# Optimization experiments

Hardware: AMD Instinct MI355X
Metric: run time of the kernel (lower is better)

Reference implementation:

```python
import jax, jax.numpy as jnp
import numpy as np

B, S, H = 1, 2048, 4096
NH, DN, DR, DV = 32, 128, 64, 128   # heads, nope dim, rope dim, v dim
QK = DN + DR                         # 192
RQ, RKV = 1536, 512
EPS = 1e-6
NEG = jnp.float32(-1e9)


def rmsnorm(x, w, eps=EPS):
    x32 = x.astype(jnp.float32)
    var = jnp.mean(x32 * x32, axis=-1, keepdims=True)
    return (x32 * jax.lax.rsqrt(var + eps)).astype(x.dtype) * w


def rope_complex(x, cos, sin):
    # x: [..., S, D]; interpret adjacent pairs as complex, multiply by e^{i*theta}
    xr, xi = x[..., 0::2], x[..., 1::2]
    or_ = xr * cos - xi * sin
    oi_ = xr * sin + xi * cos
    return jnp.stack([or_, oi_], axis=-1).reshape(x.shape)


def setup_inputs() -> dict:
    key = jax.random.key(0)
    ks = jax.random.split(key, 8)
    std = 0.02
    # RoPE angles: theta_j = pos * base^{-2j/DR}, shape [B, S, DR/2]
    inv_freq = 1.0 / (10000.0 ** (np.arange(0, DR, 2, dtype=np.float32) / DR))
    pos = np.arange(S, dtype=np.float32)
    freqs = jnp.asarray(np.broadcast_to(pos[:, None] * inv_freq[None, :], (B, S, DR // 2)))
    return {
        "hidden_states": jax.random.normal(ks[0], (B, S, H), jnp.float32),
        "freqs": freqs,
        "q_a_w": jax.random.normal(ks[1], (RQ, H), jnp.float32) * std,
        "q_a_ln_w": jnp.ones((RQ,), jnp.float32),
        "q_b_w": jax.random.normal(ks[2], (NH * QK, RQ), jnp.float32) * std,
        "kv_a_w": jax.random.normal(ks[3], (RKV + DR, H), jnp.float32) * std,
        "kv_a_ln_w": jnp.ones((RKV,), jnp.float32),
        "kv_b_w": jax.random.normal(ks[4], (NH * (DN + DV), RKV), jnp.float32) * std,
        "o_w": jax.random.normal(ks[5], (H, NH * DV), jnp.float32) * std,
    }


def reference(hidden_states, freqs, q_a_w, q_a_ln_w, q_b_w, kv_a_w, kv_a_ln_w, kv_b_w, o_w):
    b, s, _ = hidden_states.shape
    # --- low-rank Q: hidden -> q_lora_rank -> heads*(nope+rope) ---
    q = rmsnorm(hidden_states @ q_a_w.T, q_a_ln_w) @ q_b_w.T          # [B,S,NH*QK]
    q = q.reshape(b, s, NH, QK).transpose(0, 2, 1, 3)                  # [B,NH,S,QK]
    q_pass, q_rot = q[..., :DN], q[..., DN:]                           # [B,NH,S,DN],[B,NH,S,DR]
    # --- compressed KV + shared rope key ---
    ckv = hidden_states @ kv_a_w.T                                     # [B,S,RKV+DR]
    k_pass_c, k_rot = ckv[..., :RKV], ckv[..., RKV:]
    kv = rmsnorm(k_pass_c, kv_a_ln_w) @ kv_b_w.T                       # [B,S,NH*(DN+DV)]
    kv = kv.reshape(b, s, NH, DN + DV).transpose(0, 2, 1, 3)           # [B,NH,S,DN+DV]
    k_pass, v = kv[..., :DN], kv[..., DN:]
    k_rot = k_rot.reshape(b, 1, s, DR)                                 # [B,1,S,DR]
    # --- decoupled RoPE (complex form) ---
    cos = jnp.cos(freqs)[:, None]                                      # [B,1,S,DR/2]
    sin = jnp.sin(freqs)[:, None]
    q_rot = rope_complex(q_rot, cos, sin)
    k_rot = rope_complex(k_rot, cos, sin)
    k_rot = jnp.broadcast_to(k_rot, (b, NH, s, DR))
    query = jnp.concatenate([q_pass, q_rot], axis=-1)                  # [B,NH,S,QK]
    key = jnp.concatenate([k_pass, k_rot], axis=-1)
    # --- causal attention ---
    scaling = QK ** -0.5
    scores = jnp.einsum("bhqd,bhkd->bhqk", query, key) * scaling
    causal = jnp.tril(jnp.ones((s, s), bool))
    scores = jnp.where(causal, scores, NEG)
    probs = jax.nn.softmax(scores.astype(jnp.float32), axis=-1).astype(query.dtype)
    out = jnp.einsum("bhqk,bhkd->bhqd", probs, v)                      # [B,NH,S,DV]
    out = out.transpose(0, 2, 1, 3).reshape(b, s, NH * DV)
    return out @ o_w.T                                                 # [B,S,H]
```

## Files before the change

### kernel.cpp

```cpp
#include <hip/hip_runtime.h>
#define S_LEN 2048
#define HDIM 4096
#define NHEAD 32
#define QKD 192
#define RQ_ 1536
#define CKV_W 576
#define NQKV 2112
#define KVW 8192
#define QFW 6144
#define SC2F 0.1041216313667742f

typedef float f32x4 __attribute__((ext_vector_type(4)));
typedef __bf16 bf16x8 __attribute__((ext_vector_type(8)));

__device__ __forceinline__ unsigned short f2bf(float f) {
  unsigned int u = __float_as_uint(f);
  u += 0x7fffu + ((u >> 16) & 1u);
  return (unsigned short)(u >> 16);
}
__device__ __forceinline__ float b2f(unsigned short u) {
  return __uint_as_float((unsigned int)u << 16);
}
__device__ __forceinline__ float ex2(float x) { return exp2f(x); }

__device__ __forceinline__ void stage16(const void* g, void* lds_base, int lane) {
  __builtin_amdgcn_global_load_lds(
      (const __attribute__((address_space(1))) unsigned int*)g,
      (__attribute__((address_space(3))) unsigned int*)lds_base, 16, 0, 0);
}

__global__ __launch_bounds__(256) void cvt_kernel(
    const float* __restrict__ in, unsigned short* __restrict__ out, int n8) {
  int i = blockIdx.x * 256 + threadIdx.x;
  if (i >= n8) return;
  const float4* p = reinterpret_cast<const float4*>(in) + (size_t)i * 2;
  float4 a = p[0], b = p[1];
  unsigned long long lo = (unsigned long long)f2bf(a.x) | ((unsigned long long)f2bf(a.y) << 16)
      | ((unsigned long long)f2bf(a.z) << 32) | ((unsigned long long)f2bf(a.w) << 48);
  unsigned long long hi = (unsigned long long)f2bf(b.x) | ((unsigned long long)f2bf(b.y) << 16)
      | ((unsigned long long)f2bf(b.z) << 32) | ((unsigned long long)f2bf(b.w) << 48);
  unsigned long long* q = reinterpret_cast<unsigned long long*>(out) + (size_t)i * 2;
  q[0] = lo; q[1] = hi;
}

__global__ __launch_bounds__(256) void cvt2_kernel(
    const float* __restrict__ s1, int n8_1,
    const float* __restrict__ s2, unsigned short* __restrict__ out, int n8_tot) {
  int i = blockIdx.x * 256 + threadIdx.x;
  if (i >= n8_tot) return;
  const float4* p = (i < n8_1)
      ? reinterpret_cast<const float4*>(s1) + (size_t)i * 2
      : reinterpret_cast<const float4*>(s2) + (size_t)(i - n8_1) * 2;
  float4 a = p[0], b = p[1];
  unsigned long long lo = (unsigned long long)f2bf(a.x) | ((unsigned long long)f2bf(a.y) << 16)
      | ((unsigned long long)f2bf(a.z) << 32) | ((unsigned long long)f2bf(a.w) << 48);
  unsigned long long hi = (unsigned long long)f2bf(b.x) | ((unsigned long long)f2bf(b.y) << 16)
      | ((unsigned long long)f2bf(b.z) << 32) | ((unsigned long long)f2bf(b.w) << 48);
  unsigned long long* q = reinterpret_cast<unsigned long long*>(out) + (size_t)i * 2;
  q[0] = lo; q[1] = hi;
}

template<bool BF16OUT, bool SPLITK>
__global__ __launch_bounds__(256) void gemm_bf(
    const unsigned short* __restrict__ A, int lda,
    const unsigned short* __restrict__ B, int ldb,
    void* __restrict__ Cv, int ldc, int N, int K) {
  __shared__ unsigned short As[2][4][128][8];
  __shared__ unsigned short Bs[2][4][128][8];
  const int tid = threadIdx.x, lane = tid & 63, w = tid >> 6;
  const int gx = (int)gridDim.x, gy = (int)gridDim.y;
  const int nwg = gx * gy;
  int lin = (int)blockIdx.y * gx + (int)blockIdx.x;
  if ((nwg & 7) == 0) lin = (lin & 7) * (nwg >> 3) + (lin >> 3);
  const int bm = (lin % gy) * 128, bn = (lin / gy) * 128;
  const int koff = SPLITK ? (int)blockIdx.z * K : 0;
  const int wr = (w >> 1) * 64, wc = (w & 1) * 64;
  const int lg = lane >> 4, lm = lane & 15;
  f32x4 acc[4][4] = {};
  const int arow = bm + lane;
  int brow = bn + lane; if (brow >= N) brow = N - 1;

  auto STAGE = [&](int buf, int k0) {
#pragma unroll
    for (int i = 0; i < 2; ++i) {
      stage16(A + (size_t)(arow + i * 64) * lda + koff + k0 + w * 8, &As[buf][w][i * 64][0], lane);
      int br2 = brow + i * 64; if (br2 >= N) br2 = N - 1;
      stage16(B + (size_t)br2 * ldb + koff + k0 + w * 8, &Bs[buf][w][i * 64][0], lane);
    }
  };
  STAGE(0, 0);
  __syncthreads();
  int cur = 0;
  for (int k0 = 0; k0 < K; k0 += 32) {
    if (k0 + 32 < K) STAGE(cur ^ 1, k0 + 32);
    bf16x8 af[4], bf[4];
#pragma unroll
    for (int i = 0; i < 4; ++i)
      af[i] = *reinterpret_cast<const bf16x8*>(&As[cur][lg][wr + i * 16 + lm][0]);
#pragma unroll
    for (int j = 0; j < 4; ++j)
      bf[j] = *reinterpret_cast<const bf16x8*>(&Bs[cur][lg][wc + j * 16 + lm][0]);
    __builtin_amdgcn_s_setprio(1);
#pragma unroll
    for (int i = 0; i < 4; ++i)
#pragma unroll
      for (int j = 0; j < 4; ++j)
        acc[i][j] = __builtin_amdgcn_mfma_f32_16x16x32_bf16(af[i], bf[j], acc[i][j], 0, 0, 0);
    __builtin_amdgcn_s_setprio(0);
    __syncthreads();
    cur ^= 1;
  }
  size_t zoff = SPLITK ? (size_t)blockIdx.z * S_LEN * N : 0;
#pragma unroll
  for (int i = 0; i < 4; ++i)
#pragma unroll
    for (int j = 0; j < 4; ++j)
#pragma unroll
      for (int r = 0; r < 4; ++r) {
        int row = bm + wr + i * 16 + lg * 4 + r;
        int col = bn + wc + j * 16 + lm;
        if (col < N) {
          if constexpr (BF16OUT)
            ((unsigned short*)Cv)[(size_t)row * ldc + col] = f2bf(acc[i][j][r]);
          else
            ((float*)Cv)[zoff + (size_t)row * ldc + col] = acc[i][j][r];
        }
      }
}

__global__ __launch_bounds__(256) void gemm_dual(
    const unsigned short* __restrict__ A1, int lda1,
    const unsigned short* __restrict__ B1, int ldb1,
    unsigned short* __restrict__ C1, int ldc1, int K1, int nwg1,
    const unsigned short* __restrict__ A2, int lda2,
    const unsigned short* __restrict__ B2, int ldb2,
    unsigned short* __restrict__ C2, int ldc2, int K2,
    unsigned short* __restrict__ VtOut) {
  __shared__ unsigned short As[2][4][128][8];
  __shared__ unsigned short Bs[2][4][128][8];
  const int tid = threadIdx.x, lane = tid & 63, w = tid >> 6;
  const int raw = (int)blockIdx.x;
  const bool second = (raw >= nwg1);
  const int nwg = second ? ((int)gridDim.x - nwg1) : nwg1;
  int lin = second ? raw - nwg1 : raw;
  lin = (lin & 7) * (nwg >> 3) + (lin >> 3);
  const int gy = S_LEN / 128;
  const int bm = (lin % gy) * 128, bn = (lin / gy) * 128;
  const unsigned short* A = second ? A2 : A1;
  const unsigned short* B = second ? B2 : B1;
  unsigned short* C = second ? C2 : C1;
  const int lda = second ? lda2 : lda1;
  const int ldb = second ? ldb2 : ldb1;
  const int ldc = second ? ldc2 : ldc1;
  const int K = second ? K2 : K1;
  const int wr = (w >> 1) * 64, wc = (w & 1) * 64;
  const int lg = lane >> 4, lm = lane & 15;
  f32x4 acc[4][4] = {};
  const int arow = bm + lane;
  const int brow = bn + lane;

  auto STAGE = [&](int buf, int k0) {
#pragma unroll
    for (int i = 0; i < 2; ++i) {
      stage16(A + (size_t)(arow + i * 64) * lda + k0 + w * 8, &As[buf][w][i * 64][0], lane);
      stage16(B + (size_t)(brow + i * 64) * ldb + k0 + w * 8, &Bs[buf][w][i * 64][0], lane);
    }
  };
  STAGE(0, 0);
  __syncthreads();
  int cur = 0;
  for (int k0 = 0; k0 < K; k0 += 32) {
    if (k0 + 32 < K) STAGE(cur ^ 1, k0 + 32);
    bf16x8 af[4], bf[4];
#pragma unroll
    for (int i = 0; i < 4; ++i)
      af[i] = *reinterpret_cast<const bf16x8*>(&As[cur][lg][wr + i * 16 + lm][0]);
#pragma unroll
    for (int j = 0; j < 4; ++j)
      bf[j] = *reinterpret_cast<const bf16x8*>(&Bs[cur][lg][wc + j * 16 + lm][0]);
    __builtin_amdgcn_s_setprio(1);
#pragma unroll
    for (int i = 0; i < 4; ++i)
#pragma unroll
      for (int j = 0; j < 4; ++j)
        acc[i][j] = __builtin_amdgcn_mfma_f32_16x16x32_bf16(af[i], bf[j], acc[i][j], 0, 0, 0);
    __builtin_amdgcn_s_setprio(0);
    __syncthreads();
    cur ^= 1;
  }

  if (second && (bn & 128)) {
    const int h2 = bn >> 8;
#pragma unroll
    for (int i = 0; i < 4; ++i)
#pragma unroll
      for (int j = 0; j < 4; ++j) {
        int d = wc + j * 16 + lm;
        unsigned long long pk =
              (unsigned long long)f2bf(acc[i][j][0])
            | ((unsigned long long)f2bf(acc[i][j][1]) << 16)
            | ((unsigned long long)f2bf(acc[i][j][2]) << 32)
            | ((unsigned long long)f2bf(acc[i][j][3]) << 48);
        *reinterpret_cast<unsigned long long*>(
            VtOut + (size_t)(h2 * 128 + d) * S_LEN + bm + wr + i * 16 + lg * 4) = pk;
      }
    return;
  }
#pragma unroll
  for (int i = 0; i < 4; ++i)
#pragma unroll
    for (int j = 0; j < 4; ++j)
#pragma unroll
      for (int r = 0; r < 4; ++r) {
        int row = bm + wr + i * 16 + lg * 4 + r;
        int col = bn + wc + j * 16 + lm;
        C[(size_t)row * ldc + col] = f2bf(acc[i][j][r]);
      }
}

__global__ __launch_bounds__(256) void rms_fused(
    const float* __restrict__ P, const float* __restrict__ wq,
    const float* __restrict__ wkv, const float* __restrict__ freqs,
    unsigned short* __restrict__ yq, unsigned short* __restrict__ ykv,
    unsigned short* __restrict__ Kr) {
  __shared__ float red[8];
  const int row = blockIdx.x, tid = threadIdx.x;
  const float* base = P + (size_t)row * NQKV;
  float xq[6]; float ssq = 0.f;
#pragma unroll
  for (int ii = 0; ii < 6; ++ii) {
    int j = tid + ii * 256;
    float v = 0.f;
#pragma unroll
    for (int z = 0; z < 2; ++z) v += base[(size_t)z * S_LEN * NQKV + j];
    xq[ii] = v; ssq += v * v;
  }
  const float* bkv = base + RQ_;
  float x0 = 0.f, x1 = 0.f, x2 = 0.f;
#pragma unroll
  for (int z = 0; z < 2; ++z) {
    const float* b = bkv + (size_t)z * S_LEN * NQKV;
    x0 += b[tid]; x1 += b[tid + 256];
    if (tid < 64) x2 += b[tid + 512];
  }
  float sskv = x0 * x0 + x1 * x1;
#pragma unroll
  for (int off = 1; off < 64; off <<= 1) {
    ssq += __shfl_xor(ssq, off, 64);
    sskv += __shfl_xor(sskv, off, 64);
  }
  if ((tid & 63) == 0) { red[tid >> 6] = ssq; red[4 + (tid >> 6)] = sskv; }
  __syncthreads();
  float sq = rsqrtf((red[0] + red[1] + red[2] + red[3]) / (float)RQ_ + 1e-6f);
  float skv = rsqrtf((red[4] + red[5] + red[6] + red[7]) / 512.0f + 1e-6f);
  unsigned short* q = yq + (size_t)row * RQ_;
#pragma unroll
  for (int ii = 0; ii < 6; ++ii) {
    int j = tid + ii * 256;
    q[j] = f2bf(xq[ii] * sq * wq[j]);
  }
  unsigned short* k = ykv + (size_t)row * 512;
  k[tid] = f2bf(x0 * skv * wkv[tid]);
  k[tid + 256] = f2bf(x1 * skv * wkv[tid + 256]);
  if (tid < 64) {
    float part = __shfl_xor(x2, 1, 64);
    int r = tid >> 1;
    float f = freqs[(size_t)row * 32 + r];
    float c = cosf(f), sn = sinf(f);
    float out = (tid & 1) ? (part * sn + x2 * c) : (x2 * c - part * sn);
    Kr[(size_t)row * 64 + tid] = f2bf(out);
  }
}

__global__ __launch_bounds__(256) void rope_q_kernel(
    unsigned short* __restrict__ qf, const float* __restrict__ freqs) {
  int idx = blockIdx.x * 256 + threadIdx.x;
  if (idx >= NHEAD * S_LEN * 32) return;
  int r = idx & 31, s = (idx >> 5) & (S_LEN - 1), h = idx >> 16;
  unsigned short* p = qf + (size_t)s * QFW + h * QKD + 128 + 2 * r;
  float xr = b2f(p[0]), xi = b2f(p[1]);
  float f = freqs[(size_t)s * 32 + r];
  float c = cosf(f), sn = sinf(f);
  *reinterpret_cast<unsigned int*>(p) =
      (unsigned int)f2bf(xr * c - xi * sn) | ((unsigned int)f2bf(xr * sn + xi * c) << 16);
}

__global__ __launch_bounds__(256, 3) void attn_kernel(
    const unsigned short* __restrict__ Qf,
    const unsigned short* __restrict__ KV,
    const unsigned short* __restrict__ Kr,
    const unsigned short* __restrict__ Vt,
    unsigned short* __restrict__ O) {
  __shared__ unsigned short Ks[2][32 * 192];
  __shared__ unsigned short Vs[2][128 * 32];
  __shared__ unsigned short Ps[4][16 * 32];
  const int tid = threadIdx.x, lane = tid & 63, w = tid >> 6;
  const int wg = (int)blockIdx.x;
  const int lin = (wg & 7) * 128 + (wg >> 3);
  const int h = lin >> 5;
  const int qt = 31 - (lin & 31);
  const int qr0 = qt * 64 + w * 16;
  const int lg = lane >> 4, lm = lane & 15, lm7 = lane & 7;
  const unsigned short* Qh = Qf + h * QKD;
  const int hoff = h * 256;
  const unsigned short* Vh = Vt + (size_t)h * 128 * S_LEN;

  bf16x8 qf[6];
#pragma unroll
  for (int f = 0; f < 6; ++f)
    qf[f] = *reinterpret_cast<const bf16x8*>(
        Qh + (size_t)(qr0 + lm) * QFW + f * 32 + lg * 8);

  f32x4 o[8] = {};
  float l[4] = {};

  auto STAGE = [&](int b, int kp) {
#pragma unroll
    for (int i = 0; i < 3; ++i) {
      int fb = (w * 3 + i) * 64 + lane;
      int row = fb / 24;
      int blk = fb - row * 24;
      int gb = (blk & ~7) | ((blk ^ row) & 7);
      const unsigned short* src = (blk < 16)
          ? KV + (size_t)(kp + row) * KVW + hoff + gb * 8
          : Kr + (size_t)(kp + row) * 64 + (gb - 16) * 8;
      stage16(src, &Ks[b][(w * 3 + i) * 512], lane);
    }
#pragma unroll
    for (int i = 0; i < 2; ++i) {
      int fb = (w * 2 + i) * 64 + lane;
      int row = fb >> 2;
      int blk = fb & 3;
      stage16(Vh + (size_t)row * S_LEN + kp + blk * 8, &Vs[b][(w * 2 + i) * 512], lane);
    }
  };

  const int ntiles = (qt + 1) * 2;
  STAGE(0, 0);
  __syncthreads();
  int buf = 0;
  for (int ti = 0; ti < ntiles; ++ti) {
    const int kp = ti * 32;
    if (ti + 1 < ntiles) STAGE(buf ^ 1, kp + 32);
    if (kp <= qr0 + 15) {
      f32x4 sc[2] = {};
      __builtin_amdgcn_s_setprio(1);
#pragma unroll
      for (int f = 0; f < 6; ++f)
#pragma unroll
        for (int c = 0; c < 2; ++c) {
          int blk = f * 4 + lg;
          int sb = (blk & ~7) | ((blk ^ lm7) & 7);
          bf16x8 kf = *reinterpret_cast<const bf16x8*>(&Ks[buf][(c * 16 + lm) * 192 + sb * 8]);
          sc[c] = __builtin_amdgcn_mfma_f32_16x16x32_bf16(qf[f], kf, sc[c], 0, 0, 0);
        }
      __builtin_amdgcn_s_setprio(0);
      const int rb = qr0 + lg * 4;
#pragma unroll
      for (int r = 0; r < 4; ++r) {
        const int row = rb + r;
        float v0 = fmaf(sc[0][r], SC2F, -32.f); if (kp + lm > row) v0 = -1e9f;
        float v1 = fmaf(sc[1][r], SC2F, -32.f); if (kp + 16 + lm > row) v1 = -1e9f;
        float p0 = ex2(v0), p1 = ex2(v1);
        l[r] += p0 + p1;
        int pr = lg * 4 + r;
        int s3 = pr & 3;
        int b0 = lm >> 3;
        unsigned short* pp = &Ps[w][pr * 32];
        pp[((b0 ^ s3) << 3) + lm7] = f2bf(p0);
        pp[(((2 + b0) ^ s3) << 3) + lm7] = f2bf(p1);
      }
      bf16x8 pa = *reinterpret_cast<const bf16x8*>(
          &Ps[w][lm * 32 + ((lg ^ (lm & 3)) << 3)]);
      __builtin_amdgcn_s_setprio(1);
#pragma unroll
      for (int d = 0; d < 8; ++d) {
        bf16x8 vf = *reinterpret_cast<const bf16x8*>(&Vs[buf][(d * 16 + lm) * 32 + lg * 8]);
        o[d] = __builtin_amdgcn_mfma_f32_16x16x32_bf16(pa, vf, o[d], 0, 0, 0);
      }
      __builtin_amdgcn_s_setprio(0);
    }
    __syncthreads();
    buf ^= 1;
  }
#pragma unroll
  for (int r = 0; r < 4; ++r) {
    float t = l[r];
#pragma unroll
    for (int off = 1; off < 16; off <<= 1) t += __shfl_xor(t, off, 16);
    float inv = 1.0f / t;
    int row = qr0 + lg * 4 + r;
#pragma unroll
    for (int d = 0; d < 8; ++d)
      O[(size_t)row * 4096 + h * 128 + d * 16 + lm] = f2bf(o[d][r] * inv);
  }
}

extern "C" void kernel_launch(void* const* d_in, const int* in_sizes, int n_in,
                              void* d_out, int out_size, void* d_ws, size_t ws_size,
                              hipStream_t stream) {
  const float* hs = (const float*)d_in[0];
  const float* freqs = (const float*)d_in[1];
  const float* q_a_w = (const float*)d_in[2];
  const float* q_a_ln = (const float*)d_in[3];
  const float* q_b_w = (const float*)d_in[4];
  const float* kv_a_w = (const float*)d_in[5];
  const float* kv_a_ln = (const float*)d_in[6];
  const float* kv_b_w = (const float*)d_in[7];
  const float* o_w = (const float*)d_in[8];
  float* out = (float*)d_out;

  char* ws = (char*)d_ws;
  unsigned short* wslot = (unsigned short*)(ws + 0);
  unsigned short* hs_bf = (unsigned short*)(ws + 33554432);
  unsigned short* attnb = (unsigned short*)(ws + 33554432);
  float* qkv_part = (float*)(ws + 50331648);
  unsigned short* kv_bf = (unsigned short*)(ws + 50331648);
  unsigned short* qa_bf = (unsigned short*)(ws + 138412032);
  unsigned short* ckv_bf = (unsigned short*)(ws + 144703488);
  unsigned short* qfullb = (unsigned short*)(ws + 147324928);
  unsigned short* Vt = (unsigned short*)(ws + 172490752);
  unsigned short* Kr = (unsigned short*)(ws + 189267968);

  dim3 blk(256);
  auto cvt = [&](const float* src, unsigned short* dst, size_t n) {
    int n8 = (int)(n / 8);
    cvt_kernel<<<(n8 + 255) / 256, blk, 0, stream>>>(src, dst, n8);
  };
  auto cvt2 = [&](const float* s1, size_t n1, const float* s2, size_t n2,
                  unsigned short* dst) {
    int n8_1 = (int)(n1 / 8), n8_t = (int)((n1 + n2) / 8);
    cvt2_kernel<<<(n8_t + 255) / 256, blk, 0, stream>>>(s1, n8_1, s2, dst, n8_t);
  };

  cvt(hs, hs_bf, (size_t)S_LEN * HDIM);
  cvt2(q_a_w, (size_t)RQ_ * HDIM, kv_a_w, (size_t)CKV_W * HDIM, wslot);
  gemm_bf<false, true><<<dim3(17, S_LEN / 128, 2), blk, 0, stream>>>(
      hs_bf, HDIM, wslot, HDIM, qkv_part, NQKV, NQKV, HDIM / 2);
  rms_fused<<<S_LEN, blk, 0, stream>>>(qkv_part, q_a_ln, kv_a_ln, freqs,
                                       qa_bf, ckv_bf, Kr);
  cvt2(q_b_w, (size_t)QFW * RQ_, kv_b_w, (size_t)KVW * 512, wslot);
  gemm_dual<<<dim3(1792), blk, 0, stream>>>(
      qa_bf, RQ_, wslot, RQ_, qfullb, QFW, RQ_, 768,
      ckv_bf, 512, wslot + (size_t)QFW * RQ_, 512, kv_bf, KVW, 512, Vt);
  rope_q_kernel<<<(NHEAD * S_LEN * 32 + 255) / 256, blk, 0, stream>>>(qfullb, freqs);
  attn_kernel<<<dim3(1024), blk, 0, stream>>>(qfullb, kv_bf, Kr, Vt, attnb);
  cvt(o_w, wslot, (size_t)HDIM * HDIM);
  gemm_bf<false, false><<<dim3(HDIM / 128, S_LEN / 128), blk, 0, stream>>>(
      attnb, HDIM, wslot, HDIM, out, HDIM, HDIM, HDIM);
}
```

Before: 505.4 us.

## Fold o_w bf16 conversion into extra workgroups of the dual GEMM launch

Removes the standalone o_w fp32-to-bf16 conversion kernel and instead appends 256 workgroups to the gemm_dual grid that grid-stride convert o_w into a new workspace region. The aim is to overlap the memory-bound conversion with the compute-bound projection GEMMs and save one kernel launch. The converted weights get their own buffer so they are not overwritten by later use of wslot. Risk: the conversion blocks compete with GEMM tiles for bandwidth and CU slots, and the new buffer must not overlap live data such as kv_bf or the attention inputs.

```diff
diff --git a/kernel.cpp b/kernel.cpp
--- a/kernel.cpp
+++ b/kernel.cpp
@@ -134,14 +134,34 @@
     unsigned short* __restrict__ C1, int ldc1, int K1, int nwg1,
     const unsigned short* __restrict__ A2, int lda2,
     const unsigned short* __restrict__ B2, int ldb2,
-    unsigned short* __restrict__ C2, int ldc2, int K2,
-    unsigned short* __restrict__ VtOut) {
+    unsigned short* __restrict__ C2, int ldc2, int K2, int nwg2,
+    unsigned short* __restrict__ VtOut,
+    const float* __restrict__ cvt_src, unsigned short* __restrict__ cvt_dst,
+    int n8cvt) {
+  const int tid = threadIdx.x;
+  const int raw = (int)blockIdx.x;
+
+  if (raw >= nwg1 + nwg2) {
+    const int ncvt = (int)gridDim.x - nwg1 - nwg2;
+    const int stride = ncvt * 256;
+    for (int i = (raw - nwg1 - nwg2) * 256 + tid; i < n8cvt; i += stride) {
+      const float4* p = reinterpret_cast<const float4*>(cvt_src) + (size_t)i * 2;
+      float4 a = p[0], b = p[1];
+      unsigned long long lo = (unsigned long long)f2bf(a.x) | ((unsigned long long)f2bf(a.y) << 16)
+          | ((unsigned long long)f2bf(a.z) << 32) | ((unsigned long long)f2bf(a.w) << 48);
+      unsigned long long hi = (unsigned long long)f2bf(b.x) | ((unsigned long long)f2bf(b.y) << 16)
+          | ((unsigned long long)f2bf(b.z) << 32) | ((unsigned long long)f2bf(b.w) << 48);
+      unsigned long long* q = reinterpret_cast<unsigned long long*>(cvt_dst) + (size_t)i * 2;
+      q[0] = lo; q[1] = hi;
+    }
+    return;
+  }
+
   __shared__ unsigned short As[2][4][128][8];
   __shared__ unsigned short Bs[2][4][128][8];
-  const int tid = threadIdx.x, lane = tid & 63, w = tid >> 6;
-  const int raw = (int)blockIdx.x;
+  const int lane = tid & 63, w = tid >> 6;
   const bool second = (raw >= nwg1);
-  const int nwg = second ? ((int)gridDim.x - nwg1) : nwg1;
+  const int nwg = second ? nwg2 : nwg1;
   int lin = second ? raw - nwg1 : raw;
   lin = (lin & 7) * (nwg >> 3) + (lin >> 3);
   const int gy = S_LEN / 128;
@@ -416,6 +436,7 @@
   unsigned short* attnb = (unsigned short*)(ws + 33554432);
   float* qkv_part = (float*)(ws + 50331648);
   unsigned short* kv_bf = (unsigned short*)(ws + 50331648);
+  unsigned short* o_w_bf = (unsigned short*)(ws + 84934656);
   unsigned short* qa_bf = (unsigned short*)(ws + 138412032);
   unsigned short* ckv_bf = (unsigned short*)(ws + 144703488);
   unsigned short* qfullb = (unsigned short*)(ws + 147324928);
@@ -440,12 +461,12 @@
   rms_fused<<<S_LEN, blk, 0, stream>>>(qkv_part, q_a_ln, kv_a_ln, freqs,
                                        qa_bf, ckv_bf, Kr);
   cvt2(q_b_w, (size_t)QFW * RQ_, kv_b_w, (size_t)KVW * 512, wslot);
-  gemm_dual<<<dim3(1792), blk, 0, stream>>>(
+  gemm_dual<<<dim3(2048), blk, 0, stream>>>(
       qa_bf, RQ_, wslot, RQ_, qfullb, QFW, RQ_, 768,
-      ckv_bf, 512, wslot + (size_t)QFW * RQ_, 512, kv_bf, KVW, 512, Vt);
+      ckv_bf, 512, wslot + (size_t)QFW * RQ_, 512, kv_bf, KVW, 512, 1024, Vt,
+      o_w, o_w_bf, (int)((size_t)HDIM * HDIM / 8));
   rope_q_kernel<<<(NHEAD * S_LEN * 32 + 255) / 256, blk, 0, stream>>>(qfullb, freqs);
   attn_kernel<<<dim3(1024), blk, 0, stream>>>(qfullb, kv_bf, Kr, Vt, attnb);
-  cvt(o_w, wslot, (size_t)HDIM * HDIM);
   gemm_bf<false, false><<<dim3(HDIM / 128, S_LEN / 128), blk, 0, stream>>>(
-      attnb, HDIM, wslot, HDIM, out, HDIM, HDIM, HDIM);
-}
+      attnb, HDIM, o_w_bf, HDIM, out, HDIM, HDIM, HDIM);
+}
```

Result: no change. 502.3 us, median of 2 (-0.6%).
